# Kernel tuning notes

Measured on AMD Instinct MI355X. Metric: run time of the kernel, lower is better.

Reference implementation:

```python
import jax, jax.numpy as jnp
import numpy as np

B, D, FD, HW, NH, NC = 8, 384, 256, 64, 8, 4
NP = HW * HW
HD = D // NH


def _ln(x, g, b, eps=1e-5):
    m = jnp.mean(x, -1, keepdims=True)
    v = jnp.mean((x - m) ** 2, -1, keepdims=True)
    return (x - m) / jnp.sqrt(v + eps) * g + b


def _grn(x, g, b, eps=1e-6):
    # x: [B, D, H, W]; global L2 norm per channel over spatial dims
    gx = jnp.sqrt(jnp.sum(x * x, axis=(-2, -1), keepdims=True))  # [B,D,1,1]
    nx = gx / (jnp.mean(gx, axis=-3, keepdims=True) + eps)
    return (1.0 + g[:, None, None]) * (x * nx) + b[:, None, None] + x


def _adaln(x, film, W, bW, g, b):
    gb = film @ W.T + bW                       # [B, 2D]
    gamma, beta = jnp.split(gb, 2, axis=-1)
    return _grn(x, g, b) * (1.0 + gamma)[:, :, None, None] + beta[:, :, None, None]


def setup_inputs() -> dict:
    ks = jax.random.split(jax.random.key(0), 24)
    n = lambda k, s: jax.random.normal(k, s, jnp.float32)
    w = lambda k, o, i: n(k, (o, i)) * 0.02
    return {
        "image": n(ks[0], (B, D, HW, HW)),
        "film_vector": n(ks[1], (B, FD)),
        "perm": jax.random.permutation(ks[2], NP).astype(jnp.int32),
        "Wq": w(ks[3], D, D), "bq": jnp.zeros(D),
        "Wk": w(ks[4], D, D), "bk": jnp.zeros(D),
        "Wv": w(ks[5], D, D), "bv": jnp.zeros(D),
        "Wo": w(ks[6], D, D), "bo": jnp.zeros(D),
        "lnq_g": jnp.ones(D), "lnq_b": jnp.zeros(D),
        "lnk_g": jnp.ones(D), "lnk_b": jnp.zeros(D),
        "ada1_W": n(ks[7], (2 * D, FD)) * 0.001, "ada1_b": jnp.zeros(2 * D),
        "grn1_g": jnp.zeros(D), "grn1_b": jnp.zeros(D),
        "ada2_W": n(ks[8], (2 * D, FD)) * 0.001, "ada2_b": jnp.zeros(2 * D),
        "grn2_g": jnp.zeros(D), "grn2_b": jnp.zeros(D),
        "conv1_W": w(ks[9], 4 * D, D), "conv1_b": jnp.zeros(4 * D),
        "conv2_W": w(ks[10], D, 4 * D), "conv2_b": jnp.zeros(D),
        "cloud_scalar": jnp.ones(D),
        "ffn_scalar": jnp.ones(D),
        "final_scalar": jnp.ones(D) * 0.1,
        "num_clouds": NC,
    }


def reference(image, film_vector, perm, Wq, bq, Wk, bk, Wv, bv, Wo, bo,
              lnq_g, lnq_b, lnk_g, lnk_b, ada1_W, ada1_b, grn1_g, grn1_b,
              ada2_W, ada2_b, grn2_g, grn2_b, conv1_W, conv1_b, conv2_W, conv2_b,
              cloud_scalar, ffn_scalar, final_scalar, num_clouds):
    b, d, h, w = image.shape
    tp = h * w
    gs = tp // num_clouds

    # ---- cloud attention branch ----
    x = _adaln(image, film_vector, ada1_W, ada1_b, grn1_g, grn1_b)
    x_sh = x.reshape(b, d, tp)[:, :, perm]                       # shuffled pixels
    xg = x_sh.transpose(0, 2, 1).reshape(b * num_clouds, gs, d)  # [b*nc, gs, d]

    q = _ln(xg @ Wq.T + bq, lnq_g, lnq_b)
    k = _ln(xg @ Wk.T + bk, lnk_g, lnk_b)
    v = (xg @ Wv.T + bv).reshape(-1, gs, NH, HD)
    q = jax.nn.elu(q.reshape(-1, gs, NH, HD)) + 1.0
    k = jax.nn.elu(k.reshape(-1, gs, NH, HD)) + 1.0

    kv = jnp.einsum('bnhd,bnhe->bhde', k, v)                 # [b*nc, H, hd, hd]
    ksum = k.sum(axis=1)                                      # [b*nc, H, hd]
    num = jnp.einsum('bqhd,bhde->bqhe', q, kv)
    den = jnp.einsum('bqhd,bhd->bqh', q, ksum)[..., None] + 1e-8
    ao = (num / den).reshape(-1, gs, d) @ Wo.T + bo           # [b*nc, gs, d]

    ao = ao.reshape(b, num_clouds, gs, d).transpose(0, 3, 1, 2).reshape(b, d, tp)
    inv_perm = jnp.argsort(perm)
    ao = ao[:, :, inv_perm].reshape(b, d, h, w)

    wi = image + ao * cloud_scalar[:, None, None]

    # ---- FFN branch (1x1 convs) ----
    x2 = _adaln(wi, film_vector, ada2_W, ada2_b, grn2_g, grn2_b)
    h1 = jax.nn.silu(jnp.einsum('bdhw,ed->behw', x2, conv1_W) + conv1_b[:, None, None])
    fo = jnp.einsum('behw,de->bdhw', h1, conv2_W) + conv2_b[:, None, None]
    wi = wi + fo * ffn_scalar[:, None, None]

    return image + wi * final_scalar[:, None, None]
```

## Files before the change

kernel.cpp:

```cpp
#include <hip/hip_runtime.h>
#include <hip/hip_bf16.h>
#include <math.h>

#define BB      8
#define DD      384
#define FDIM    256
#define NPIX    4096
#define NHEAD   8
#define NCLOUD  4
#define HDIM    48
#define GSZ     1024
#define TT      (BB*NPIX)
#define DHID    (4*DD)
#define TD      1152

typedef __hip_bfloat16 bf16;
typedef __attribute__((ext_vector_type(8))) short bf16x8;
typedef __attribute__((ext_vector_type(4))) float f32x4;
typedef __attribute__((ext_vector_type(2))) unsigned int u32x2;

__device__ __forceinline__ float b2f(bf16 x){ return __bfloat162float(x); }
__device__ __forceinline__ bf16  f2b(float x){ return __float2bfloat16(x); }
__device__ __forceinline__ float lo2f(unsigned u){ union{unsigned i; float f;} c; c.i = u << 16; return c.f; }
__device__ __forceinline__ float hi2f(unsigned u){ union{unsigned i; float f;} c; c.i = u & 0xffff0000u; return c.f; }
__device__ __forceinline__ unsigned short f2bs(float x){ bf16 b = f2b(x); return *(unsigned short*)&b; }
__device__ __forceinline__ unsigned pack2(float a, float b){
    return (unsigned)f2bs(a) | ((unsigned)f2bs(b) << 16);
}

#if defined(__has_builtin)
#if __has_builtin(__builtin_amdgcn_global_load_lds)
#define USE_GLL 1
#endif
#endif
#ifndef USE_GLL
#define USE_GLL 0
#endif

typedef __attribute__((address_space(1))) void gas_t;
typedef __attribute__((address_space(3))) void las_t;
__device__ __forceinline__ void gload16(const void* g, void* l){
#if USE_GLL
    __builtin_amdgcn_global_load_lds((gas_t*)(void*)g, (las_t*)l, 16, 0, 0);
#else
    *(bf16x8*)l = *(const bf16x8*)g;
#endif
}

__device__ __forceinline__ float block_sum(float v, float* sm, int nthreads){
    #pragma unroll
    for (int o = 32; o > 0; o >>= 1) v += __shfl_down(v, o, 64);
    int nw = nthreads >> 6;
    __syncthreads();
    if ((threadIdx.x & 63) == 0) sm[threadIdx.x >> 6] = v;
    __syncthreads();
    float s = sm[0];
    for (int i = 1; i < nw; i++) s += sm[i];
    return s;
}

#define WSEG 147456
#define WBIG 589824
__global__ void prologue(const float* Wq, const float* Wk, const float* Wv, const float* Wo,
                         const float* W1, const float* W2, bf16* wb,
                         const float* film, const float* ada1_W, const float* ada1_b,
                         const float* ada2_W, const float* ada2_b, float* gb1, float* gb2,
                         const int* perm, int* invp,
                         const float* bq, const float* bk, const float* bv, float* bqkv,
                         float* gxsq, float* gxsq2){
    int blk = blockIdx.x, tid = threadIdx.x;
    if (blk < 6912){
        int i = blk*256 + tid;
        float v;
        if      (i <   WSEG) v = Wq[i];
        else if (i < 2*WSEG) v = Wk[i -   WSEG];
        else if (i < 3*WSEG) v = Wv[i - 2*WSEG];
        else if (i < 4*WSEG) v = Wo[i - 3*WSEG];
        else if (i < 4*WSEG + WBIG) v = W1[i - 4*WSEG];
        else v = W2[i - 4*WSEG - WBIG];
        wb[i] = f2b(v);
    } else if (blk < 6960){
        int idx = (blk-6912)*256 + tid;
        int which = idx / (BB*768);
        int r = idx % (BB*768);
        int bb = r / 768, j = r % 768;
        const float* W = which ? ada2_W : ada1_W;
        const float* bi = which ? ada2_b : ada1_b;
        const float* f = film + bb*FDIM;
        const float* w = W + (size_t)j*FDIM;
        float s = 0.f;
        for (int i = 0; i < FDIM; i++) s += f[i]*w[i];
        (which ? gb2 : gb1)[bb*768 + j] = s + bi[j];
    } else if (blk < 6976){
        int i = (blk-6960)*256 + tid;
        if (i < NPIX) invp[perm[i]] = i;
    } else if (blk < 6981){
        int i = (blk-6976)*256 + tid;
        if (i < 384) bqkv[i] = bq[i];
        else if (i < 768) bqkv[i] = bk[i-384];
        else if (i < 1152) bqkv[i] = bv[i-768];
    } else {
        int i = (blk-6981)*256 + tid;
        if (i < BB*DD){ gxsq[i] = 0.f; gxsq2[i] = 0.f; }
    }
}

__global__ void prep1(const float* img, bf16* imgT, float* gxsq){
    __shared__ float tile[32][33];
    __shared__ float red[32][8];
    int b = blockIdx.z, p0 = blockIdx.x*32, d0 = blockIdx.y*32;
    int tx = threadIdx.x, ty = threadIdx.y;
    #pragma unroll
    for (int i = 0; i < 32; i += 8)
        tile[ty+i][tx] = img[((size_t)b*DD + d0+ty+i)*NPIX + p0+tx];
    __syncthreads();
    #pragma unroll
    for (int i = 0; i < 32; i += 8){
        int p = p0 + ty + i;
        imgT[((size_t)(b<<12) + p)*DD + d0+tx] = f2b(tile[tx][ty+i]);
    }
    float s = 0.f;
    #pragma unroll
    for (int k = 0; k < 4; k++){ float v = tile[tx][ty*4 + k]; s += v*v; }
    red[tx][ty] = s;
    __syncthreads();
    if (ty == 0){
        float t2 = 0.f;
        #pragma unroll
        for (int k = 0; k < 8; k++) t2 += red[tx][k];
        atomicAdd(&gxsq[b*DD + d0+tx], t2);
    }
}

template<bool SQ>
__global__ void grn_nx(const float* gin, float* nx){
    __shared__ float sm[6];
    int b = blockIdx.x; int d = threadIdx.x;
    float g = gin[b*DD + d];
    if (SQ) g = sqrtf(g);
    float tot = block_sum(g, sm, 384);
    nx[b*DD + d] = g / (tot/(float)DD + 1e-6f);
}

__global__ __launch_bounds__(256) void adaln1_tok(const bf16* imgT, const float* nx,
                        const float* gg, const float* gbv, const float* gb,
                        const int* invp, bf16* xt){
    int t = blockIdx.x*4 + (threadIdx.x >> 6);
    int lane = threadIdx.x & 63;
    int b = t >> 12, p = t & 4095;
    int j = invp[p];
    const unsigned* src = (const unsigned*)(imgT + (size_t)t*DD);
    unsigned* dst = (unsigned*)(xt + ((size_t)(b<<12) + j)*DD);
    int d0 = lane*6;
    const float* nxp = nx + b*DD + d0;
    const float* g1 = gb + b*768 + d0;
    const float* g2 = gb + b*768 + 384 + d0;
    #pragma unroll
    for (int i = 0; i < 3; i++){
        unsigned u = src[lane*3 + i];
        float v0 = lo2f(u), v1 = hi2f(u);
        int dd0 = 2*i, dd1 = 2*i+1;
        float r0 = ((1.f + gg[d0+dd0])*(v0*nxp[dd0]) + gbv[d0+dd0] + v0)*(1.f + g1[dd0]) + g2[dd0];
        float r1 = ((1.f + gg[d0+dd1])*(v1*nxp[dd1]) + gbv[d0+dd1] + v1)*(1.f + g1[dd1]) + g2[dd1];
        dst[lane*3 + i] = pack2(r0, r1);
    }
}

__global__ __launch_bounds__(256) void adaln2_tok(const bf16* wi, const float* nx,
                        const float* gg, const float* gbv, const float* gb, bf16* xout){
    int t = blockIdx.x*4 + (threadIdx.x >> 6);
    int lane = threadIdx.x & 63;
    int b = t >> 12;
    const unsigned* src = (const unsigned*)(wi + (size_t)t*DD);
    unsigned* dst = (unsigned*)(xout + (size_t)t*DD);
    int d0 = lane*6;
    const float* nxp = nx + b*DD + d0;
    const float* g1 = gb + b*768 + d0;
    const float* g2 = gb + b*768 + 384 + d0;
    #pragma unroll
    for (int i = 0; i < 3; i++){
        unsigned u = src[lane*3 + i];
        float v0 = lo2f(u), v1 = hi2f(u);
        int dd0 = 2*i, dd1 = 2*i+1;
        float r0 = ((1.f + gg[d0+dd0])*(v0*nxp[dd0]) + gbv[d0+dd0] + v0)*(1.f + g1[dd0]) + g2[dd0];
        float r1 = ((1.f + gg[d0+dd1])*(v1*nxp[dd1]) + gbv[d0+dd1] + v1)*(1.f + g1[dd1]) + g2[dd1];
        dst[lane*3 + i] = pack2(r0, r1);
    }
}

template<int EPI>
__global__ __launch_bounds__(256) void gemm_mfma(const bf16* __restrict__ A,
                          const bf16* __restrict__ W,
                          const float* __restrict__ bias,
                          bf16* __restrict__ C,
                          int M, int N, int K, const int* __restrict__ rowmap,
                          const bf16* __restrict__ imgT, const float* __restrict__ csc){
    __shared__ short lds_[8192];
    int tid  = threadIdx.x;
    int lane = tid & 63, wid = tid >> 6;
    int quad = lane >> 4, l16 = lane & 15;
    int wm = (wid >> 1) * 64, wn = (wid & 1) * 64;

    int v = blockIdx.y * gridDim.x + blockIdx.x;
    int xcd = v & 7, ii = v >> 3;
    int by = xcd * 32 + ii / gridDim.x;
    int bx = ii % gridDim.x;
    int m0 = by * 128, n0 = bx * 128;

    const bf16* sp[4]; short* lp[4];
    #pragma unroll
    for (int it = 0; it < 4; it++){
        int s = tid + it*256;
        int half = s >> 9;
        int r = (s >> 2) & 127;
        int seg = s & 3;
        sp[it] = (half ? W + (size_t)(n0 + r)*K : A + (size_t)(m0 + r)*K) + seg*8;
        lp[it] = lds_ + (size_t)s*8;
    }

    f32x4 acc[4][4] = {};
    for (int k0 = 0; k0 < K; k0 += 32){
        #pragma unroll
        for (int it = 0; it < 4; it++) gload16(sp[it] + k0, lp[it]);
        __syncthreads();
        bf16x8 af[4], wf[4];
        #pragma unroll
        for (int t = 0; t < 4; t++){
            af[t] = *(const bf16x8*)(void*)(lds_ + (wm + t*16 + l16)*32 + quad*8);
            wf[t] = *(const bf16x8*)(void*)(lds_ + 4096 + (wn + t*16 + l16)*32 + quad*8);
        }
        #pragma unroll
        for (int i = 0; i < 4; i++)
            #pragma unroll
            for (int j2 = 0; j2 < 4; j2++)
                acc[i][j2] = __builtin_amdgcn_mfma_f32_16x16x32_bf16(wf[j2], af[i], acc[i][j2], 0, 0, 0);
        __syncthreads();
    }
    int nbase = n0 + wn + quad*4;
    f32x4 bsv[4], csv[4];
    #pragma unroll
    for (int j2 = 0; j2 < 4; j2++) bsv[j2] = *(const f32x4*)(bias + nbase + j2*16);
    if (EPI == 2){
        #pragma unroll
        for (int j2 = 0; j2 < 4; j2++) csv[j2] = *(const f32x4*)(csc + nbase + j2*16);
    }
    #pragma unroll
    for (int i = 0; i < 4; i++){
        int row = m0 + wm + i*16 + l16;
        int grow = rowmap ? ((row & ~4095) | rowmap[row & 4095]) : row;
        bf16* cp = C + (size_t)grow*N + nbase;
        const bf16* ip = imgT + (size_t)grow*DD + nbase;
        #pragma unroll
        for (int j2 = 0; j2 < 4; j2++){
            float v0 = acc[i][j2][0] + bsv[j2][0];
            float v1 = acc[i][j2][1] + bsv[j2][1];
            float v2 = acc[i][j2][2] + bsv[j2][2];
            float v3 = acc[i][j2][3] + bsv[j2][3];
            if (EPI == 1){
                v0 = v0 / (1.f + __expf(-v0));
                v1 = v1 / (1.f + __expf(-v1));
                v2 = v2 / (1.f + __expf(-v2));
                v3 = v3 / (1.f + __expf(-v3));
            }
            if (EPI == 2){
                u32x2 iw = *(const u32x2*)(void*)(ip + j2*16);
                v0 = lo2f(iw.x) + v0*csv[j2][0];
                v1 = hi2f(iw.x) + v1*csv[j2][1];
                v2 = lo2f(iw.y) + v2*csv[j2][2];
                v3 = hi2f(iw.y) + v3*csv[j2][3];
            }
            u32x2 st;
            st.x = pack2(v0, v1);
            st.y = pack2(v2, v3);
            *(u32x2*)(void*)(cp + j2*16) = st;
        }
    }
}

__global__ __launch_bounds__(256) void ln_elu_qk(bf16* qkv,
                        const float* gq, const float* bq2,
                        const float* gk, const float* bk2){
    int r = blockIdx.x*4 + (threadIdx.x >> 6);
    int lane = threadIdx.x & 63;
    int t = r >> 1, which = r & 1;
    unsigned* row32 = (unsigned*)(qkv + (size_t)t*TD + which*384);
    const float* g = which ? gk : gq;
    const float* b = which ? bk2 : bq2;
    unsigned u[3];
    #pragma unroll
    for (int i = 0; i < 3; i++) u[i] = row32[lane*3 + i];
    float vv[6];
    #pragma unroll
    for (int i = 0; i < 3; i++){ vv[2*i] = lo2f(u[i]); vv[2*i+1] = hi2f(u[i]); }
    float s = 0.f;
    #pragma unroll
    for (int i = 0; i < 6; i++) s += vv[i];
    #pragma unroll
    for (int o = 32; o > 0; o >>= 1) s += __shfl_xor(s, o, 64);
    float mean = s / (float)DD;
    float s2 = 0.f;
    #pragma unroll
    for (int i = 0; i < 6; i++){ float d = vv[i]-mean; s2 += d*d; }
    #pragma unroll
    for (int o = 32; o > 0; o >>= 1) s2 += __shfl_xor(s2, o, 64);
    float rstd = rsqrtf(s2/(float)DD + 1e-5f);
    int d0 = lane*6;
    #pragma unroll
    for (int i = 0; i < 3; i++){
        float y0 = (vv[2*i]-mean)*rstd*g[d0+2*i] + b[d0+2*i];
        float y1 = (vv[2*i+1]-mean)*rstd*g[d0+2*i+1] + b[d0+2*i+1];
        y0 = (y0 > 0.f) ? y0 : expm1f(y0);
        y1 = (y1 > 0.f) ? y1 : expm1f(y1);
        row32[lane*3 + i] = pack2(y0 + 1.f, y1 + 1.f);
    }
}

__global__ __launch_bounds__(256) void kv_ksum_part(const bf16* qkv, float* kvp, float* ksp){
    int bch = blockIdx.x >> 3, sub = blockIdx.x & 7;
    int bc = bch >> 3, h = bch & 7;
    __shared__ float ks[16][49];
    __shared__ float vs[16][49];
    int eg = (threadIdx.x >> 4) * 3;
    int fg = (threadIdx.x & 15) * 3;
    float acc[3][3] = {};
    float ksacc[3] = {};
    int nbase = bc*GSZ + sub*128;
    for (int n0 = 0; n0 < 128; n0 += 16){
        for (int i = threadIdx.x; i < 16*48; i += 256){
            int n = i/48, e = i%48;
            size_t base = (size_t)(nbase + n0 + n)*TD + h*HDIM;
            ks[n][e] = b2f(qkv[base + 384 + e]);
            vs[n][e] = b2f(qkv[base + 768 + e]);
        }
        __syncthreads();
        #pragma unroll 4
        for (int n = 0; n < 16; n++){
            float ka[3], vb[3];
            #pragma unroll
            for (int i = 0; i < 3; i++){ ka[i] = ks[n][eg+i]; vb[i] = vs[n][fg+i]; }
            #pragma unroll
            for (int i = 0; i < 3; i++)
                #pragma unroll
                for (int j = 0; j < 3; j++)
                    acc[i][j] += ka[i]*vb[j];
            if ((threadIdx.x & 15) == 0){
                #pragma unroll
                for (int i = 0; i < 3; i++) ksacc[i] += ka[i];
            }
        }
        __syncthreads();
    }
    float* kvo = kvp + (size_t)blockIdx.x*2304;
    #pragma unroll
    for (int i = 0; i < 3; i++)
        #pragma unroll
        for (int j = 0; j < 3; j++)
            kvo[(eg+i)*48 + fg+j] = acc[i][j];
    if ((threadIdx.x & 15) == 0){
        #pragma unroll
        for (int i = 0; i < 3; i++) ksp[(size_t)blockIdx.x*48 + eg+i] = ksacc[i];
    }
}

__global__ void kv_reduce(const float* kvp, const float* ksp, float* kv, float* ksum){
    int idx = blockIdx.x*256 + threadIdx.x;
    if (idx < 256*2304){
        int bch = idx / 2304, r = idx - bch*2304;
        const float* p = kvp + (size_t)bch*8*2304 + r;
        float s = 0.f;
        #pragma unroll
        for (int u = 0; u < 8; u++) s += p[u*2304];
        kv[idx] = s;
    } else if (idx < 256*2304 + 256*48){
        int k2 = idx - 256*2304;
        int bch = k2 / 48, r = k2 - bch*48;
        const float* p = ksp + (size_t)bch*8*48 + r;
        float s = 0.f;
        #pragma unroll
        for (int u = 0; u < 8; u++) s += p[u*48];
        ksum[k2] = s;
    }
}

__global__ __launch_bounds__(256) void attn_apply(const bf16* __restrict__ qkv,
                                                  const float* __restrict__ kv,
                                                  const float* __restrict__ ksum,
                                                  bf16* __restrict__ out){
    __shared__ __align__(16) bf16 Wm[64][72];
    int bch = blockIdx.x >> 2, rs = blockIdx.x & 3;
    int bc = bch >> 3, h = bch & 7;
    int tid = threadIdx.x;
    int lane = tid & 63, w = tid >> 6;
    int l16 = lane & 15, quad = lane >> 4;

    for (int i = tid; i < 64*72; i += 256) ((unsigned short*)Wm)[i] = 0;
    __syncthreads();
    const float* kvh = kv + (size_t)bch*(HDIM*HDIM);
    for (int i = tid; i < HDIM*HDIM; i += 256){
        int e = i / HDIM, f = i - e*HDIM;
        Wm[f][e] = f2b(kvh[i]);
    }
    if (tid < HDIM) Wm[HDIM][tid] = f2b(ksum[(size_t)bch*HDIM + tid]);
    __syncthreads();

    bf16x8 bw[4][2];
    #pragma unroll
    for (int n = 0; n < 4; n++){
        bw[n][0] = *(const bf16x8*)(void*)&Wm[n*16 + l16][quad*8];
        bw[n][1] = *(const bf16x8*)(void*)&Wm[n*16 + l16][32 + quad*8];
    }

    int rowbase0 = bc*GSZ + rs*256 + w*64;
    #pragma unroll
    for (int frag = 0; frag < 4; frag++){
        int arow = rowbase0 + frag*16 + l16;
        const bf16* qp = qkv + (size_t)arow*TD + h*HDIM;
        bf16x8 a0 = *(const bf16x8*)(void*)(qp + quad*8);
        bf16x8 a1 = {};
        if (quad < 2) a1 = *(const bf16x8*)(void*)(qp + 32 + quad*8);
        f32x4 acc[4] = {};
        #pragma unroll
        for (int n = 0; n < 4; n++){
            acc[n] = __builtin_amdgcn_mfma_f32_16x16x32_bf16(a0, bw[n][0], acc[n], 0, 0, 0);
            acc[n] = __builtin_amdgcn_mfma_f32_16x16x32_bf16(a1, bw[n][1], acc[n], 0, 0, 0);
        }
        int orow0 = rowbase0 + frag*16 + quad*4;
        #pragma unroll
        for (int r = 0; r < 4; r++){
            float den = __shfl(acc[3][r], quad*16, 64);
            float inv = 1.f / (den + 1e-8f);
            bf16* op = out + (size_t)(orow0 + r)*DD + h*HDIM + l16;
            op[0]  = f2b(acc[0][r]*inv);
            op[16] = f2b(acc[1][r]*inv);
            op[32] = f2b(acc[2][r]*inv);
        }
    }
}

__global__ __launch_bounds__(256) void colsq(const bf16* wi, float* gxsq2){
    __shared__ float red[4][DD];
    int wave = threadIdx.x >> 6, lane = threadIdx.x & 63;
    int t0 = blockIdx.x*128 + wave*32;
    int b = (blockIdx.x*128) >> 12;
    int d0 = lane*6;
    float acc[6] = {};
    for (int it = 0; it < 32; it++){
        const unsigned* pw = (const unsigned*)(wi + (size_t)(t0 + it)*DD);
        #pragma unroll
        for (int i = 0; i < 3; i++){
            unsigned u = pw[lane*3 + i];
            float v0 = lo2f(u), v1 = hi2f(u);
            acc[2*i]   += v0*v0;
            acc[2*i+1] += v1*v1;
        }
    }
    #pragma unroll
    for (int i = 0; i < 6; i++) red[wave][d0+i] = acc[i];
    __syncthreads();
    for (int d = threadIdx.x; d < DD; d += 256){
        float s = red[0][d] + red[1][d] + red[2][d] + red[3][d];
        atomicAdd(&gxsq2[b*DD + d], s);
    }
}

__global__ void final_out(const float* img, const bf16* wi, const bf16* fot,
                          const float* ffs, const float* fins, float* out){
    __shared__ float tile[32][33];
    int b = blockIdx.z, p0 = blockIdx.x*32, d0 = blockIdx.y*32;
    int tx = threadIdx.x, ty = threadIdx.y;
    #pragma unroll
    for (int i = 0; i < 32; i += 8){
        size_t t = (size_t)(b<<12) + p0+ty+i;
        tile[ty+i][tx] = b2f(wi[t*DD + d0+tx]) + b2f(fot[t*DD + d0+tx])*ffs[d0+tx];
    }
    __syncthreads();
    #pragma unroll
    for (int i = 0; i < 32; i += 8){
        int d = d0 + ty + i;
        size_t o = ((size_t)b*DD + d)*NPIX + p0+tx;
        out[o] = img[o] + tile[tx][ty+i]*fins[d];
    }
}

extern "C" void kernel_launch(void* const* d_in, const int* in_sizes, int n_in,
                              void* d_out, int out_size, void* d_ws, size_t ws_size,
                              hipStream_t stream){
    const float* image   = (const float*)d_in[0];
    const float* film    = (const float*)d_in[1];
    const int*   perm    = (const int*)  d_in[2];
    const float* Wq      = (const float*)d_in[3];
    const float* bq      = (const float*)d_in[4];
    const float* Wk      = (const float*)d_in[5];
    const float* bk      = (const float*)d_in[6];
    const float* Wv      = (const float*)d_in[7];
    const float* bv      = (const float*)d_in[8];
    const float* Wo      = (const float*)d_in[9];
    const float* bo      = (const float*)d_in[10];
    const float* lnq_g   = (const float*)d_in[11];
    const float* lnq_b   = (const float*)d_in[12];
    const float* lnk_g   = (const float*)d_in[13];
    const float* lnk_b   = (const float*)d_in[14];
    const float* ada1_W  = (const float*)d_in[15];
    const float* ada1_b  = (const float*)d_in[16];
    const float* grn1_g  = (const float*)d_in[17];
    const float* grn1_b  = (const float*)d_in[18];
    const float* ada2_W  = (const float*)d_in[19];
    const float* ada2_b  = (const float*)d_in[20];
    const float* grn2_g  = (const float*)d_in[21];
    const float* grn2_b  = (const float*)d_in[22];
    const float* conv1_W = (const float*)d_in[23];
    const float* conv1_b = (const float*)d_in[24];
    const float* conv2_W = (const float*)d_in[25];
    const float* conv2_b = (const float*)d_in[26];
    const float* cs      = (const float*)d_in[27];
    const float* ffs     = (const float*)d_in[28];
    const float* fins    = (const float*)d_in[29];
    float* out = (float*)d_out;

    char* m = (char*)d_ws;
    float* gb1     = (float*)m;  m += (size_t)BB*768*4;
    float* gb2     = (float*)m;  m += (size_t)BB*768*4;
    int*   invp    = (int*)m;    m += (size_t)NPIX*4;
    float* gxsq    = (float*)m;  m += (size_t)BB*DD*4;
    float* gxsq2   = (float*)m;  m += (size_t)BB*DD*4;
    float* nx      = (float*)m;  m += (size_t)BB*DD*4;
    float* kvbuf   = (float*)m;  m += (size_t)256*HDIM*HDIM*4;
    float* ksumbuf = (float*)m;  m += (size_t)256*HDIM*4;
    float* kvp     = (float*)m;  m += (size_t)2048*2304*4;
    float* ksp     = (float*)m;  m += (size_t)2048*48*4;
    float* bqkv    = (float*)m;  m += (size_t)TD*4;
    bf16*  wb      = (bf16*)m;   m += (size_t)(4*WSEG + 2*WBIG)*2;
    bf16*  wqkv = wb;
    bf16*  wbo  = wb + 3*WSEG;
    bf16*  wb1  = wb + 4*WSEG, *wb2 = wb + 4*WSEG + WBIG;
    bf16* imgT = (bf16*)m;       m += (size_t)TT*DD*2;
    bf16* qkv = (bf16*)m;        m += (size_t)TT*TD*2;
    bf16* obf = (bf16*)m;        m += (size_t)TT*DD*2;
    bf16* abf = (bf16*)m;        m += (size_t)TT*DD*2;
    bf16* wi  = (bf16*)m;        m += (size_t)TT*DD*2;
    bf16* H1  = qkv;
    (void)obf;

    prologue<<<6993, 256, 0, stream>>>(Wq, Wk, Wv, Wo, conv1_W, conv2_W, wb,
                                       film, ada1_W, ada1_b, ada2_W, ada2_b, gb1, gb2,
                                       perm, invp, bq, bk, bv, bqkv, gxsq, gxsq2);

    prep1<<<dim3(128,12,BB), dim3(32,8), 0, stream>>>(image, imgT, gxsq);
    grn_nx<true><<<BB, DD, 0, stream>>>(gxsq, nx);
    adaln1_tok<<<TT/4, 256, 0, stream>>>(imgT, nx, grn1_g, grn1_b, gb1, invp, abf);
    gemm_mfma<0><<<dim3(9,256), 256, 0, stream>>>(abf, wqkv, bqkv, qkv, TT, TD, DD, nullptr, nullptr, nullptr);
    ln_elu_qk<<<2*TT/4, 256, 0, stream>>>(qkv, lnq_g, lnq_b, lnk_g, lnk_b);
    kv_ksum_part<<<2048, 256, 0, stream>>>(qkv, kvp, ksp);
    kv_reduce<<<2352, 256, 0, stream>>>(kvp, ksp, kvbuf, ksumbuf);
    attn_apply<<<1024, 256, 0, stream>>>(qkv, kvbuf, ksumbuf, abf);
    gemm_mfma<2><<<dim3(3,256), 256, 0, stream>>>(abf, wbo, bo, wi, TT, DD, DD, perm, imgT, cs);
    colsq<<<BB*32, 256, 0, stream>>>(wi, gxsq2);

    grn_nx<true><<<BB, DD, 0, stream>>>(gxsq2, nx);
    adaln2_tok<<<TT/4, 256, 0, stream>>>(wi, nx, grn2_g, grn2_b, gb2, abf);
    gemm_mfma<1><<<dim3(12,256), 256, 0, stream>>>(abf, wb1, conv1_b, H1, TT, DHID, DD, nullptr, nullptr, nullptr);
    gemm_mfma<0><<<dim3(3,256), 256, 0, stream>>>(H1, wb2, conv2_b, abf, TT, DD, DHID, nullptr, nullptr, nullptr);
    final_out<<<dim3(128,12,BB), dim3(32,8), 0, stream>>>(image, wi, abf, ffs, fins, out);
}
```

Before: 556.3 us.

## Double-buffer GEMM weight tiles in LDS, load A fragments directly to registers

Restructures the MFMA GEMM main loop into a two-stage software pipeline. Weight tiles are prefetched into alternating LDS buffers with an XOR swizzle to reduce bank conflicts. A fragments are loaded straight from global memory into registers rather than staged through LDS. The goal is to overlap global loads with MFMA work and halve LDS traffic per step, at the cost of more registers and redundant global reads of A across the two N-warps.

```diff
diff --git a/kernel.cpp b/kernel.cpp
--- a/kernel.cpp
+++ b/kernel.cpp
@@ -207,33 +207,68 @@
     int bx = ii % gridDim.x;
     int m0 = by * 128, n0 = bx * 128;
 
-    const bf16* sp[4]; short* lp[4];
-    #pragma unroll
-    for (int it = 0; it < 4; it++){
+    const bf16* sp[2]; int lof[2];
+    #pragma unroll
+    for (int it = 0; it < 2; it++){
         int s = tid + it*256;
-        int half = s >> 9;
-        int r = (s >> 2) & 127;
-        int seg = s & 3;
-        sp[it] = (half ? W + (size_t)(n0 + r)*K : A + (size_t)(m0 + r)*K) + seg*8;
-        lp[it] = lds_ + (size_t)s*8;
-    }
+        int r = s >> 2;
+        int seg = (s & 3) ^ ((s >> 3) & 3);
+        sp[it] = W + (size_t)(n0 + r)*K + seg*8;
+        lof[it] = s*8;
+    }
+    int xorv = (quad ^ ((l16 >> 1) & 3)) * 8;
+
+    const bf16* ap[4];
+    #pragma unroll
+    for (int t = 0; t < 4; t++)
+        ap[t] = A + (size_t)(m0 + wm + t*16 + l16)*K + quad*8;
+
+    #pragma unroll
+    for (int it = 0; it < 2; it++) gload16(sp[it], lds_ + lof[it]);
+    bf16x8 af0[4], af1[4];
+    #pragma unroll
+    for (int t = 0; t < 4; t++) af0[t] = *(const bf16x8*)(void*)(ap[t]);
+    __syncthreads();
 
     f32x4 acc[4][4] = {};
-    for (int k0 = 0; k0 < K; k0 += 32){
-        #pragma unroll
-        for (int it = 0; it < 4; it++) gload16(sp[it] + k0, lp[it]);
+    for (int k0 = 0; k0 < K; k0 += 64){
+        {
+            int kn = k0 + 32;
+            #pragma unroll
+            for (int it = 0; it < 2; it++) gload16(sp[it] + kn, lds_ + 4096 + lof[it]);
+            #pragma unroll
+            for (int t = 0; t < 4; t++) af1[t] = *(const bf16x8*)(void*)(ap[t] + kn);
+        }
+        {
+            const short* w_ = lds_ + (wn + l16)*32 + xorv;
+            bf16x8 wf[4];
+            #pragma unroll
+            for (int t = 0; t < 4; t++) wf[t] = *(const bf16x8*)(void*)(w_ + t*512);
+            #pragma unroll
+            for (int i = 0; i < 4; i++)
+                #pragma unroll
+                for (int j2 = 0; j2 < 4; j2++)
+                    acc[i][j2] = __builtin_amdgcn_mfma_f32_16x16x32_bf16(wf[j2], af0[i], acc[i][j2], 0, 0, 0);
+        }
         __syncthreads();
-        bf16x8 af[4], wf[4];
-        #pragma unroll
-        for (int t = 0; t < 4; t++){
-            af[t] = *(const bf16x8*)(void*)(lds_ + (wm + t*16 + l16)*32 + quad*8);
-            wf[t] = *(const bf16x8*)(void*)(lds_ + 4096 + (wn + t*16 + l16)*32 + quad*8);
-        }
-        #pragma unroll
-        for (int i = 0; i < 4; i++)
-            #pragma unroll
-            for (int j2 = 0; j2 < 4; j2++)
-                acc[i][j2] = __builtin_amdgcn_mfma_f32_16x16x32_bf16(wf[j2], af[i], acc[i][j2], 0, 0, 0);
+        if (k0 + 64 < K){
+            int kn = k0 + 64;
+            #pragma unroll
+            for (int it = 0; it < 2; it++) gload16(sp[it] + kn, lds_ + lof[it]);
+            #pragma unroll
+            for (int t = 0; t < 4; t++) af0[t] = *(const bf16x8*)(void*)(ap[t] + kn);
+        }
+        {
+            const short* w_ = lds_ + 4096 + (wn + l16)*32 + xorv;
+            bf16x8 wf[4];
+            #pragma unroll
+            for (int t = 0; t < 4; t++) wf[t] = *(const bf16x8*)(void*)(w_ + t*512);
+            #pragma unroll
+            for (int i = 0; i < 4; i++)
+                #pragma unroll
+                for (int j2 = 0; j2 < 4; j2++)
+                    acc[i][j2] = __builtin_amdgcn_mfma_f32_16x16x32_bf16(wf[j2], af1[i], acc[i][j2], 0, 0, 0);
+        }
         __syncthreads();
     }
     int nbase = n0 + wn + quad*4;
```

Measured after the change: 672.8 us. 1.21x slower.
